# Kernel tuning notes

Measured on AMD Instinct MI355X. Metric: run time of the kernel, lower is better.

## Reference

```python
import jax, jax.numpy as jnp
import numpy as np

MASK_NUM = 64  # band half-width, matches init kwarg


def setup_inputs() -> dict:
    key = jax.random.key(0)
    kq, kk, kv = jax.random.split(key, 3)
    B, T, D = 4, 4096, 64
    queries = jax.random.normal(kq, (B, T, D), dtype=jnp.float32)
    keys = jax.random.normal(kk, (B, T, D), dtype=jnp.float32)
    values = jax.random.normal(kv, (B, T, D), dtype=jnp.float32)
    mask = jnp.ones((B, T), dtype=jnp.int32)
    return {"queries": queries, "keys": keys, "values": values, "mask": mask}


def _attn(queries, keys, values, mask):
    B, T, D = queries.shape
    scale = jnp.sqrt(jnp.asarray(D, dtype=queries.dtype))
    # scores: [B, T, T]
    scores = jnp.einsum("btd,bsd->bts", queries, keys) / scale
    # band mask |i-j| <= MASK_NUM, shape [T, T]
    idx = jnp.arange(T)
    band = jnp.abs(idx[:, None] - idx[None, :]) <= MASK_NUM
    mask_b = mask.astype(bool)
    mask_i = mask_b[:, :, None]  # [B, T, 1] (query positions)
    mask_j = mask_b[:, None, :]  # [B, 1, T] (key positions)
    # original: band*mask_j + (1-mask_i)*mask_j, cast to bool
    # == mask_j & (band | ~mask_i)
    allowed = mask_j & (band[None] | ~mask_i)
    scores = jnp.where(allowed, scores, -jnp.inf)
    probs = jax.nn.softmax(scores, axis=-1)
    return jnp.einsum("bts,bsd->btd", probs, values)


def reference(queries, keys, values, mask):
    return _attn(queries, keys, values, mask)
```

## Files before the change

kernel.cpp:

```cpp
#include <hip/hip_runtime.h>
#include <math.h>


typedef __attribute__((ext_vector_type(8))) short bf16x8;
typedef __attribute__((ext_vector_type(4))) float f32x4;

constexpr int kT    = 4096;
constexpr int kD    = 64;
constexpr int kBand = 64;
constexpr int KP    = 72;
constexpr int VP    = 264;

__device__ __forceinline__ short f2bf(float x) {
    return (short)((__float_as_uint(x) + 0x8000u) >> 16);
}
__device__ __forceinline__ unsigned pack2(float lo, float hi) {
    return (unsigned)(unsigned short)f2bf(lo) |
           ((unsigned)(unsigned short)f2bf(hi) << 16);
}

__global__ __launch_bounds__(256, 1) void mfma_band_attn(
    const float* __restrict__ Q,
    const float* __restrict__ K,
    const float* __restrict__ V,
    const int*   __restrict__ M,
    float* __restrict__ O)
{
    __shared__ short Ks[192 * KP];
    __shared__ short Vs[64 * VP];
    __shared__ int   wflag[4];

    const int tid  = threadIdx.x;
    const int lane = tid & 63;
    const int wid  = tid >> 6;
    const int blk  = blockIdx.x;
    const int b    = blk >> 6;
    const int tB   = (blk & 63) << 6;
    const int tw   = tB + 16 * wid;
    const int h    = lane >> 4;
    const int q    = lane & 15;

    const float* Qg = Q + (size_t)b * kT * kD;
    const float* Kg = K + (size_t)b * kT * kD;
    const float* Vg = V + (size_t)b * kT * kD;
    const int*   mb = M + b * kT;

    int mk_win = 1, mk_q = 1;
    {
        int ka = tB - 64 + tid;
        if (tid < 192 && (unsigned)ka < (unsigned)kT) mk_win = mb[ka];
        if (tid < 64) mk_q = mb[tB + tid];
    }
    float4 qa0, qa1, qb0, qb1;
    {
        const float* qp = Qg + (size_t)(tw + q) * kD + 8 * h;
        qa0 = *(const float4*)(qp + 0);
        qa1 = *(const float4*)(qp + 4);
        qb0 = *(const float4*)(qp + 32);
        qb1 = *(const float4*)(qp + 36);
    }
    float4 kreg[12];
    #pragma unroll
    for (int i = 0; i < 12; ++i) {
        const int idx = i * 256 + tid;
        const int u   = idx >> 4;
        const int dc  = (idx & 15) << 2;
        int ka = tB - 64 + u;
        ka = ka < 0 ? 0 : (ka > kT - 1 ? kT - 1 : ka);
        kreg[i] = *(const float4*)(Kg + (size_t)ka * kD + dc);
    }
    const int va_ = lane >> 4;
    const int vc_ = lane & 15;
    float4 vA[6], vB[6];
    #pragma unroll
    for (int i = 0; i < 6; ++i) {
        const int u = 48 * wid + 8 * i + 2 * va_;
        int ka0 = tB - 64 + u;
        int ka1 = ka0 + 1;
        ka0 = ka0 < 0 ? 0 : (ka0 > kT - 1 ? kT - 1 : ka0);
        ka1 = ka1 < 0 ? 0 : (ka1 > kT - 1 ? kT - 1 : ka1);
        vA[i] = *(const float4*)(Vg + (size_t)ka0 * kD + 4 * vc_);
        vB[i] = *(const float4*)(Vg + (size_t)ka1 * kD + 4 * vc_);
    }

    int ok = (mk_win && mk_q) ? 1 : 0;
    ok = __all(ok);
    if (lane == 0) wflag[wid] = ok;

    bf16x8 qf0, qf1;
    qf0[0] = f2bf(qa0.x * 0.125f); qf0[1] = f2bf(qa0.y * 0.125f);
    qf0[2] = f2bf(qa0.z * 0.125f); qf0[3] = f2bf(qa0.w * 0.125f);
    qf0[4] = f2bf(qa1.x * 0.125f); qf0[5] = f2bf(qa1.y * 0.125f);
    qf0[6] = f2bf(qa1.z * 0.125f); qf0[7] = f2bf(qa1.w * 0.125f);
    qf1[0] = f2bf(qb0.x * 0.125f); qf1[1] = f2bf(qb0.y * 0.125f);
    qf1[2] = f2bf(qb0.z * 0.125f); qf1[3] = f2bf(qb0.w * 0.125f);
    qf1[4] = f2bf(qb1.x * 0.125f); qf1[5] = f2bf(qb1.y * 0.125f);
    qf1[6] = f2bf(qb1.z * 0.125f); qf1[7] = f2bf(qb1.w * 0.125f);

    #pragma unroll
    for (int i = 0; i < 12; ++i) {
        const int idx = i * 256 + tid;
        const int u   = idx >> 4;
        const int dc  = (idx & 15) << 2;
        const float4 f = kreg[i];
        *(uint2*)&Ks[u * KP + (dc ^ ((u & 3) << 3))] =
            make_uint2(pack2(f.x, f.y), pack2(f.z, f.w));
    }
    #pragma unroll
    for (int i = 0; i < 6; ++i) {
        const int u = 48 * wid + 8 * i + 2 * va_;
        #pragma unroll
        for (int t = 0; t < 4; ++t) {
            const int dd = 4 * vc_ + t;
            const int sw = (dd + (dd >> 3)) & 7;
            const int pos = u ^ (sw << 3);
            const float lo = (t == 0) ? vA[i].x : (t == 1) ? vA[i].y
                           : (t == 2) ? vA[i].z : vA[i].w;
            const float hi = (t == 0) ? vB[i].x : (t == 1) ? vB[i].y
                           : (t == 2) ? vB[i].z : vB[i].w;
            *(unsigned int*)&Vs[dd * VP + pos] = pack2(lo, hi);
        }
    }
    #pragma unroll
    for (int i = 0; i < 9; ++i) {
        const int idx = i * 256 + tid;
        const int row = idx / 36;
        const int col = idx - row * 36;
        *(unsigned int*)&Vs[row * VP + 192 + 2 * col] = 0u;
    }
    __syncthreads();

    if (wflag[0] && wflag[1] && wflag[2] && wflag[3]) {
        f32x4 acc[10];
        #pragma unroll
        for (int t = 0; t < 10; ++t) acc[t] = (f32x4){0.f, 0.f, 0.f, 0.f};

        #pragma unroll
        for (int t = 0; t < 9; ++t) {
            const int u  = 16 * wid + 16 * t + q;
            const short* kr = &Ks[u * KP];
            const int x  = (u & 3) << 3;
            const bf16x8 ka0 = *(const bf16x8*)(kr + ((8 * h) ^ x));
            const bf16x8 ka1 = *(const bf16x8*)(kr + ((32 + 8 * h) ^ x));
            acc[t] = __builtin_amdgcn_mfma_f32_16x16x32_bf16(ka0, qf0, acc[t], 0, 0, 0);
            acc[t] = __builtin_amdgcn_mfma_f32_16x16x32_bf16(ka1, qf1, acc[t], 0, 0, 0);
        }

        const int base = tB - 64 + 16 * wid;
        float mx = -1e30f;
        #pragma unroll
        for (int t = 0; t < 9; ++t) {
            #pragma unroll
            for (int r = 0; r < 4; ++r) {
                const int kk = 16 * t + 4 * h + r;
                const int ka = base + kk;
                const bool val = ((unsigned)(kk - q) <= 2u * kBand) &&
                                 ((unsigned)ka < (unsigned)kT);
                const float sc = val ? acc[t][r] : -1e30f;
                acc[t][r] = sc;
                mx = fmaxf(mx, sc);
            }
        }
        mx = fmaxf(mx, __shfl_xor(mx, 16, 64));
        mx = fmaxf(mx, __shfl_xor(mx, 32, 64));
        float lsum = 0.f;
        #pragma unroll
        for (int t = 0; t < 9; ++t) {
            #pragma unroll
            for (int r = 0; r < 4; ++r) {
                const float w = __expf(acc[t][r] - mx);
                acc[t][r] = w;
                lsum += w;
            }
        }
        lsum += __shfl_xor(lsum, 16, 64);
        lsum += __shfl_xor(lsum, 32, 64);

        f32x4 oacc[4];
        #pragma unroll
        for (int dt = 0; dt < 4; ++dt) oacc[dt] = (f32x4){0.f, 0.f, 0.f, 0.f};

        #pragma unroll
        for (int ks = 0; ks < 5; ++ks) {
            bf16x8 pf;
            #pragma unroll
            for (int j = 0; j < 8; ++j) {
                const int srcl = 16 * (2 * (h & 1) + (j >> 2)) + q;
                const float vlo = __shfl(acc[2 * ks][j & 3], srcl, 64);
                const float vhi = __shfl(acc[2 * ks + 1][j & 3], srcl, 64);
                pf[j] = f2bf((h < 2) ? vlo : vhi);
            }
            #pragma unroll
            for (int dt = 0; dt < 4; ++dt) {
                const int d  = 16 * dt + q;
                const int sw = (d + (d >> 3)) & 7;
                const int u0 = (16 * wid + 32 * ks + 8 * h) ^ (sw << 3);
                const bf16x8 vf = *(const bf16x8*)&Vs[d * VP + u0];
                oacc[dt] = __builtin_amdgcn_mfma_f32_16x16x32_bf16(vf, pf, oacc[dt], 0, 0, 0);
            }
        }

        const float inv = 1.0f / lsum;
        float* Ob = O + (size_t)(b * kT + tw + q) * kD;
        #pragma unroll
        for (int dt = 0; dt < 4; ++dt) {
            float4 o;
            o.x = oacc[dt][0] * inv; o.y = oacc[dt][1] * inv;
            o.z = oacc[dt][2] * inv; o.w = oacc[dt][3] * inv;
            *(float4*)(Ob + 16 * dt + 4 * h) = o;
        }
        return;
    }

    const int g8 = lane >> 3;
    const int r8 = lane & 7;
    for (int qq = 0; qq < 16; ++qq) {
        const int t  = tw + qq;
        const int qm = mb[t];
        const float* qp = Qg + (size_t)t * kD + 8 * r8;
        float4 q0 = *(const float4*)qp;
        float4 q1 = *(const float4*)(qp + 4);
        q0.x *= 0.125f; q0.y *= 0.125f; q0.z *= 0.125f; q0.w *= 0.125f;
        q1.x *= 0.125f; q1.y *= 0.125f; q1.z *= 0.125f; q1.w *= 0.125f;
        int lo, hi;
        if (qm) {
            lo = t - kBand; if (lo < 0) lo = 0;
            hi = t + kBand; if (hi > kT - 1) hi = kT - 1;
        } else {
            lo = 0; hi = kT - 1;
        }
        float m = -1e30f, l = 0.f;
        float4 a0 = make_float4(0.f, 0.f, 0.f, 0.f), a1 = a0;
        for (int s = lo + g8; s <= hi; s += 8) {
            const float* kr = Kg + (size_t)s * kD + 8 * r8;
            const float4 k0 = *(const float4*)kr;
            const float4 k1 = *(const float4*)(kr + 4);
            float d = q0.x * k0.x + q0.y * k0.y + q0.z * k0.z + q0.w * k0.w
                    + q1.x * k1.x + q1.y * k1.y + q1.z * k1.z + q1.w * k1.w;
            d += __shfl_xor(d, 1, 64);
            d += __shfl_xor(d, 2, 64);
            d += __shfl_xor(d, 4, 64);
            if (mb[s]) {
                if (d > m) {
                    const float scl = __expf(m - d);
                    l *= scl;
                    a0.x *= scl; a0.y *= scl; a0.z *= scl; a0.w *= scl;
                    a1.x *= scl; a1.y *= scl; a1.z *= scl; a1.w *= scl;
                    m = d;
                }
                const float w = __expf(d - m);
                const float* vr = Vg + (size_t)s * kD + 8 * r8;
                const float4 v0 = *(const float4*)vr;
                const float4 v1 = *(const float4*)(vr + 4);
                l += w;
                a0.x += w * v0.x; a0.y += w * v0.y; a0.z += w * v0.z; a0.w += w * v0.w;
                a1.x += w * v1.x; a1.y += w * v1.y; a1.z += w * v1.z; a1.w += w * v1.w;
            }
        }
        float Mx = m;
        Mx = fmaxf(Mx, __shfl_xor(Mx, 8, 64));
        Mx = fmaxf(Mx, __shfl_xor(Mx, 16, 64));
        Mx = fmaxf(Mx, __shfl_xor(Mx, 32, 64));
        const float scl = __expf(m - Mx);
        l *= scl;
        a0.x *= scl; a0.y *= scl; a0.z *= scl; a0.w *= scl;
        a1.x *= scl; a1.y *= scl; a1.z *= scl; a1.w *= scl;
        #pragma unroll
        for (int off = 8; off <= 32; off <<= 1) {
            l += __shfl_xor(l, off, 64);
            a0.x += __shfl_xor(a0.x, off, 64); a0.y += __shfl_xor(a0.y, off, 64);
            a0.z += __shfl_xor(a0.z, off, 64); a0.w += __shfl_xor(a0.w, off, 64);
            a1.x += __shfl_xor(a1.x, off, 64); a1.y += __shfl_xor(a1.y, off, 64);
            a1.z += __shfl_xor(a1.z, off, 64); a1.w += __shfl_xor(a1.w, off, 64);
        }
        if (g8 == 0) {
            const float inv = 1.0f / l;
            float* orow = O + (size_t)(b * kT + t) * kD + 8 * r8;
            float4 o0, o1;
            o0.x = a0.x * inv; o0.y = a0.y * inv; o0.z = a0.z * inv; o0.w = a0.w * inv;
            o1.x = a1.x * inv; o1.y = a1.y * inv; o1.z = a1.z * inv; o1.w = a1.w * inv;
            *(float4*)orow       = o0;
            *(float4*)(orow + 4) = o1;
        }
    }
}

extern "C" void kernel_launch(void* const* d_in, const int* in_sizes, int n_in,
                              void* d_out, int out_size, void* d_ws, size_t ws_size,
                              hipStream_t stream) {
    const float* q    = (const float*)d_in[0];
    const float* k    = (const float*)d_in[1];
    const float* v    = (const float*)d_in[2];
    const int*   mask = (const int*)d_in[3];
    float*       out  = (float*)d_out;
    (void)d_ws; (void)ws_size; (void)in_sizes; (void)n_in; (void)out_size;

    dim3 grid(256);
    dim3 block(256);
    mfma_band_attn<<<grid, block, 0, stream>>>(q, k, v, mask, out);
}
```

Baseline: 12.02 us.

## Split key range across two wave halves and merge softmax partials in LDS

Doubles the block to 512 threads. Each query tile is now handled by two waves that each cover half of the key band, and their partial outputs, sums and maxima are combined through shared memory using a flash-style rescale. Block indices are also remapped so that consecutive blocks interleave across batches. The aim is more parallelism per CU and shorter per-wave dependency chains, at the cost of an extra barrier and an LDS merge step.

```diff
diff --git a/kernel.cpp b/kernel.cpp
--- a/kernel.cpp
+++ b/kernel.cpp
@@ -19,7 +19,7 @@
            ((unsigned)(unsigned short)f2bf(hi) << 16);
 }
 
-__global__ __launch_bounds__(256, 1) void mfma_band_attn(
+__global__ __launch_bounds__(512, 2) void mfma_band_attn(
     const float* __restrict__ Q,
     const float* __restrict__ K,
     const float* __restrict__ V,
@@ -28,15 +28,20 @@
 {
     __shared__ short Ks[192 * KP];
     __shared__ short Vs[64 * VP];
-    __shared__ int   wflag[4];
+    __shared__ int   wflag[8];
 
     const int tid  = threadIdx.x;
     const int lane = tid & 63;
     const int wid  = tid >> 6;
-    const int blk  = blockIdx.x;
+    const int qg   = wid & 3;
+    const int hf   = wid >> 2;
+
+    const int phys = blockIdx.x;
+    const int blk  = (phys & 7) * 32 + (phys >> 3);
+
     const int b    = blk >> 6;
     const int tB   = (blk & 63) << 6;
-    const int tw   = tB + 16 * wid;
+    const int tw   = tB + 16 * qg;
     const int h    = lane >> 4;
     const int q    = lane & 15;
 
@@ -59,10 +64,10 @@
         qb0 = *(const float4*)(qp + 32);
         qb1 = *(const float4*)(qp + 36);
     }
-    float4 kreg[12];
-    #pragma unroll
-    for (int i = 0; i < 12; ++i) {
-        const int idx = i * 256 + tid;
+    float4 kreg[6];
+    #pragma unroll
+    for (int i = 0; i < 6; ++i) {
+        const int idx = i * 512 + tid;
         const int u   = idx >> 4;
         const int dc  = (idx & 15) << 2;
         int ka = tB - 64 + u;
@@ -71,10 +76,10 @@
     }
     const int va_ = lane >> 4;
     const int vc_ = lane & 15;
-    float4 vA[6], vB[6];
-    #pragma unroll
-    for (int i = 0; i < 6; ++i) {
-        const int u = 48 * wid + 8 * i + 2 * va_;
+    float4 vA[3], vB[3];
+    #pragma unroll
+    for (int i = 0; i < 3; ++i) {
+        const int u = 24 * wid + 8 * i + 2 * va_;
         int ka0 = tB - 64 + u;
         int ka1 = ka0 + 1;
         ka0 = ka0 < 0 ? 0 : (ka0 > kT - 1 ? kT - 1 : ka0);
@@ -98,8 +103,8 @@
     qf1[6] = f2bf(qb1.z * 0.125f); qf1[7] = f2bf(qb1.w * 0.125f);
 
     #pragma unroll
-    for (int i = 0; i < 12; ++i) {
-        const int idx = i * 256 + tid;
+    for (int i = 0; i < 6; ++i) {
+        const int idx = i * 512 + tid;
         const int u   = idx >> 4;
         const int dc  = (idx & 15) << 2;
         const float4 f = kreg[i];
@@ -107,8 +112,8 @@
             make_uint2(pack2(f.x, f.y), pack2(f.z, f.w));
     }
     #pragma unroll
-    for (int i = 0; i < 6; ++i) {
-        const int u = 48 * wid + 8 * i + 2 * va_;
+    for (int i = 0; i < 3; ++i) {
+        const int u = 24 * wid + 8 * i + 2 * va_;
         #pragma unroll
         for (int t = 0; t < 4; ++t) {
             const int dd = 4 * vc_ + t;
@@ -122,55 +127,68 @@
         }
     }
     #pragma unroll
-    for (int i = 0; i < 9; ++i) {
-        const int idx = i * 256 + tid;
-        const int row = idx / 36;
-        const int col = idx - row * 36;
-        *(unsigned int*)&Vs[row * VP + 192 + 2 * col] = 0u;
+    for (int i = 0; i < 5; ++i) {
+        const int idx = i * 512 + tid;
+        if (idx < 2304) {
+            const int row = idx / 36;
+            const int col = idx - row * 36;
+            *(unsigned int*)&Vs[row * VP + 192 + 2 * col] = 0u;
+        }
     }
     __syncthreads();
 
-    if (wflag[0] && wflag[1] && wflag[2] && wflag[3]) {
-        f32x4 acc[10];
-        #pragma unroll
-        for (int t = 0; t < 10; ++t) acc[t] = (f32x4){0.f, 0.f, 0.f, 0.f};
-
-        #pragma unroll
-        for (int t = 0; t < 9; ++t) {
-            const int u  = 16 * wid + 16 * t + q;
-            const short* kr = &Ks[u * KP];
-            const int x  = (u & 3) << 3;
-            const bf16x8 ka0 = *(const bf16x8*)(kr + ((8 * h) ^ x));
-            const bf16x8 ka1 = *(const bf16x8*)(kr + ((32 + 8 * h) ^ x));
-            acc[t] = __builtin_amdgcn_mfma_f32_16x16x32_bf16(ka0, qf0, acc[t], 0, 0, 0);
-            acc[t] = __builtin_amdgcn_mfma_f32_16x16x32_bf16(ka1, qf1, acc[t], 0, 0, 0);
-        }
-
-        const int base = tB - 64 + 16 * wid;
+    const bool fast = wflag[0] && wflag[1] && wflag[2] && wflag[3] &&
+                      wflag[4] && wflag[5] && wflag[6] && wflag[7];
+    if (fast) {
+        const int tb = hf ? 4 : 0;
+        const int nt = hf ? 5 : 4;
+
+        f32x4 acc[6];
+        #pragma unroll
+        for (int t = 0; t < 6; ++t) acc[t] = (f32x4){0.f, 0.f, 0.f, 0.f};
+
+        #pragma unroll
+        for (int t = 0; t < 6; ++t) {
+            if (t < nt) {
+                const int u  = 16 * qg + 16 * (tb + t) + q;
+                const short* kr = &Ks[u * KP];
+                const int x  = (u & 3) << 3;
+                const bf16x8 ka0 = *(const bf16x8*)(kr + ((8 * h) ^ x));
+                const bf16x8 ka1 = *(const bf16x8*)(kr + ((32 + 8 * h) ^ x));
+                acc[t] = __builtin_amdgcn_mfma_f32_16x16x32_bf16(ka0, qf0, acc[t], 0, 0, 0);
+                acc[t] = __builtin_amdgcn_mfma_f32_16x16x32_bf16(ka1, qf1, acc[t], 0, 0, 0);
+            }
+        }
+
+        const int base = tB - 64 + 16 * qg;
         float mx = -1e30f;
         #pragma unroll
-        for (int t = 0; t < 9; ++t) {
-            #pragma unroll
-            for (int r = 0; r < 4; ++r) {
-                const int kk = 16 * t + 4 * h + r;
-                const int ka = base + kk;
-                const bool val = ((unsigned)(kk - q) <= 2u * kBand) &&
-                                 ((unsigned)ka < (unsigned)kT);
-                const float sc = val ? acc[t][r] : -1e30f;
-                acc[t][r] = sc;
-                mx = fmaxf(mx, sc);
+        for (int t = 0; t < 6; ++t) {
+            if (t < nt) {
+                #pragma unroll
+                for (int r = 0; r < 4; ++r) {
+                    const int kk = 16 * (tb + t) + 4 * h + r;
+                    const int ka = base + kk;
+                    const bool val = ((unsigned)(kk - q) <= 2u * kBand) &&
+                                     ((unsigned)ka < (unsigned)kT);
+                    const float sc = val ? acc[t][r] : -1e30f;
+                    acc[t][r] = sc;
+                    mx = fmaxf(mx, sc);
+                }
             }
         }
         mx = fmaxf(mx, __shfl_xor(mx, 16, 64));
         mx = fmaxf(mx, __shfl_xor(mx, 32, 64));
         float lsum = 0.f;
         #pragma unroll
-        for (int t = 0; t < 9; ++t) {
-            #pragma unroll
-            for (int r = 0; r < 4; ++r) {
-                const float w = __expf(acc[t][r] - mx);
-                acc[t][r] = w;
-                lsum += w;
+        for (int t = 0; t < 6; ++t) {
+            if (t < nt) {
+                #pragma unroll
+                for (int r = 0; r < 4; ++r) {
+                    const float w = __expf(acc[t][r] - mx);
+                    acc[t][r] = w;
+                    lsum += w;
+                }
             }
         }
         lsum += __shfl_xor(lsum, 16, 64);
@@ -180,42 +198,69 @@
         #pragma unroll
         for (int dt = 0; dt < 4; ++dt) oacc[dt] = (f32x4){0.f, 0.f, 0.f, 0.f};
 
-        #pragma unroll
-        for (int ks = 0; ks < 5; ++ks) {
-            bf16x8 pf;
-            #pragma unroll
-            for (int j = 0; j < 8; ++j) {
-                const int srcl = 16 * (2 * (h & 1) + (j >> 2)) + q;
-                const float vlo = __shfl(acc[2 * ks][j & 3], srcl, 64);
-                const float vhi = __shfl(acc[2 * ks + 1][j & 3], srcl, 64);
-                pf[j] = f2bf((h < 2) ? vlo : vhi);
-            }
+        const int nks = hf ? 3 : 2;
+        #pragma unroll
+        for (int s5 = 0; s5 < 3; ++s5) {
+            if (s5 < nks) {
+                const int ks = (hf ? 2 : 0) + s5;
+                bf16x8 pf;
+                #pragma unroll
+                for (int j = 0; j < 8; ++j) {
+                    const int srcl = 16 * (2 * (h & 1) + (j >> 2)) + q;
+                    const float vlo = __shfl(acc[2 * s5][j & 3], srcl, 64);
+                    const float vhi = __shfl(acc[2 * s5 + 1][j & 3], srcl, 64);
+                    pf[j] = f2bf((h < 2) ? vlo : vhi);
+                }
+                #pragma unroll
+                for (int dt = 0; dt < 4; ++dt) {
+                    const int d  = 16 * dt + q;
+                    const int sw = (d + (d >> 3)) & 7;
+                    const int u0 = (16 * qg + 32 * ks + 8 * h) ^ (sw << 3);
+                    const bf16x8 vf = *(const bf16x8*)&Vs[d * VP + u0];
+                    oacc[dt] = __builtin_amdgcn_mfma_f32_16x16x32_bf16(vf, pf, oacc[dt], 0, 0, 0);
+                }
+            }
+        }
+
+        __syncthreads();
+        float* mrg = (float*)Ks;
+        if (hf) {
+            float* p = mrg + ((size_t)(qg * 64 + lane)) * 18;
             #pragma unroll
             for (int dt = 0; dt < 4; ++dt) {
-                const int d  = 16 * dt + q;
-                const int sw = (d + (d >> 3)) & 7;
-                const int u0 = (16 * wid + 32 * ks + 8 * h) ^ (sw << 3);
-                const bf16x8 vf = *(const bf16x8*)&Vs[d * VP + u0];
-                oacc[dt] = __builtin_amdgcn_mfma_f32_16x16x32_bf16(vf, pf, oacc[dt], 0, 0, 0);
-            }
-        }
-
-        const float inv = 1.0f / lsum;
-        float* Ob = O + (size_t)(b * kT + tw + q) * kD;
-        #pragma unroll
-        for (int dt = 0; dt < 4; ++dt) {
-            float4 o;
-            o.x = oacc[dt][0] * inv; o.y = oacc[dt][1] * inv;
-            o.z = oacc[dt][2] * inv; o.w = oacc[dt][3] * inv;
-            *(float4*)(Ob + 16 * dt + 4 * h) = o;
+                p[4 * dt + 0] = oacc[dt][0]; p[4 * dt + 1] = oacc[dt][1];
+                p[4 * dt + 2] = oacc[dt][2]; p[4 * dt + 3] = oacc[dt][3];
+            }
+            p[16] = lsum;
+            p[17] = mx;
+        }
+        __syncthreads();
+        if (!hf) {
+            const float* p = mrg + ((size_t)(qg * 64 + lane)) * 18;
+            const float l2  = p[16];
+            const float mx2 = p[17];
+            const float Mx  = fmaxf(mx, mx2);
+            const float e1  = __expf(mx  - Mx);
+            const float e2  = __expf(mx2 - Mx);
+            const float inv = 1.0f / (lsum * e1 + l2 * e2);
+            float* Ob = O + (size_t)(b * kT + tw + q) * kD;
+            #pragma unroll
+            for (int dt = 0; dt < 4; ++dt) {
+                float4 o;
+                o.x = (oacc[dt][0] * e1 + p[4 * dt + 0] * e2) * inv;
+                o.y = (oacc[dt][1] * e1 + p[4 * dt + 1] * e2) * inv;
+                o.z = (oacc[dt][2] * e1 + p[4 * dt + 2] * e2) * inv;
+                o.w = (oacc[dt][3] * e1 + p[4 * dt + 3] * e2) * inv;
+                *(float4*)(Ob + 16 * dt + 4 * h) = o;
+            }
         }
         return;
     }
 
     const int g8 = lane >> 3;
     const int r8 = lane & 7;
-    for (int qq = 0; qq < 16; ++qq) {
-        const int t  = tw + qq;
+    for (int qq = 0; qq < 8; ++qq) {
+        const int t  = tB + 8 * wid + qq;
         const int qm = mb[t];
         const float* qp = Qg + (size_t)t * kD + 8 * r8;
         float4 q0 = *(const float4*)qp;
@@ -296,6 +341,6 @@
     (void)d_ws; (void)ws_size; (void)in_sizes; (void)n_in; (void)out_size;
 
     dim3 grid(256);
-    dim3 block(256);
+    dim3 block(512);
     mfma_band_attn<<<grid, block, 0, stream>>>(q, k, v, mask, out);
 }
```

Result: no change. 12.16 us (+1.2%).
